# Performance work log

Measured on AMD Instinct MI355X. Metric: run time of the kernel, lower is better.

## Reference

```python
import jax, jax.numpy as jnp
import numpy as np

# Module config: RoDAlignMax(aligned_height=9, aligned_width=9, spatial_scale=0.25)
# Internally RoDAlignFunction is called with aligned_height+1, aligned_width+1,
# then max_pool2d(kernel=2, stride=1) shrinks each spatial dim by 1.
AH, AW = 10, 10          # pre-pool sampling grid (aligned_{h,w} + 1)
SPATIAL_SCALE = 0.25


def _rod_align(features, rois, ah, aw, scale):
    """RoDAlign: uniform bilinear sampling grid over the WHOLE feature map,
    with samples falling INSIDE the ROI zeroed out (region-of-discard).
    features: [B,C,H,W], rois: [R,5]=(batch_ind,x1,y1,x2,y2) -> [R,C,ah,aw]."""
    B, C, H, W = features.shape
    dt = features.dtype
    bidx = rois[:, 0].astype(jnp.int32)                              # [R]
    x1 = rois[:, 1] * scale
    y1 = rois[:, 2] * scale
    x2 = rois[:, 3] * scale
    y2 = rois[:, 4] * scale
    # uniform grid spanning the full feature map
    h = jnp.arange(ah, dtype=dt) * ((H - 1.0) / (ah - 1.0))          # [AH]
    w = jnp.arange(aw, dtype=dt) * ((W - 1.0) / (aw - 1.0))          # [AW]
    h0 = jnp.minimum(jnp.floor(h), H - 2).astype(jnp.int32)
    w0 = jnp.minimum(jnp.floor(w), W - 2).astype(jnp.int32)
    hr = (h - h0.astype(dt))[:, None, None]                          # [AH,1,1]
    wr = (w - w0.astype(dt))[None, :, None]                          # [1,AW,1]
    b = bidx[:, None, None]                                          # [R,1,1]
    hi0 = h0[None, :, None]; hi1 = hi0 + 1                           # [1,AH,1]
    wi0 = w0[None, None, :]; wi1 = wi0 + 1                           # [1,1,AW]
    # four corner gathers; advanced idx dims go first -> [R,AH,AW,C]
    ul = features[b, :, hi0, wi0]
    ur = features[b, :, hi0, wi1]
    dl = features[b, :, hi1, wi0]
    dr = features[b, :, hi1, wi1]
    out = (ul * (1 - hr) * (1 - wr) + ur * (1 - hr) * wr
           + dl * hr * (1 - wr) + dr * hr * wr)                      # [R,AH,AW,C]
    # zero samples inside the ROI (the kept crop region is discarded)
    in_h = (h[None, :] >= y1[:, None]) & (h[None, :] <= y2[:, None])  # [R,AH]
    in_w = (w[None, :] >= x1[:, None]) & (w[None, :] <= x2[:, None])  # [R,AW]
    inside = in_h[:, :, None] & in_w[:, None, :]                      # [R,AH,AW]
    out = jnp.where(inside[..., None], jnp.zeros((), dt), out)
    return jnp.transpose(out, (0, 3, 1, 2))                           # [R,C,AH,AW]


def _maxpool2x2_s1(x):
    # max_pool2d(kernel_size=2, stride=1) on [..., H, W]
    return jnp.maximum(jnp.maximum(x[..., :-1, :-1], x[..., :-1, 1:]),
                       jnp.maximum(x[..., 1:, :-1], x[..., 1:, 1:]))


def setup_inputs() -> dict:
    key = jax.random.key(0)
    k1, k2, k3, k4, k5 = jax.random.split(key, 5)
    B, C, H, W = 4, 256, 64, 64
    R = 2048
    img = H / SPATIAL_SCALE  # 256.0, input-image coordinate extent
    features = jax.random.normal(k1, (B, C, H, W), dtype=jnp.float32)
    bidx = jax.random.randint(k2, (R,), 0, B).astype(jnp.float32)
    x1 = jax.random.uniform(k3, (R,), dtype=jnp.float32) * (img * 0.5)
    y1 = jax.random.uniform(k4, (R,), dtype=jnp.float32) * (img * 0.5)
    wh = jax.random.uniform(k5, (R, 2), dtype=jnp.float32) * (img * 0.45) + img * 0.05
    x2 = jnp.minimum(x1 + wh[:, 0], img - 1.0)
    y2 = jnp.minimum(y1 + wh[:, 1], img - 1.0)
    rois = jnp.stack([bidx, x1, y1, x2, y2], axis=1)  # [R,5]
    return {"features": features, "rois": rois}


def reference(features, rois):
    x = _rod_align(features, rois, AH, AW, SPATIAL_SCALE)  # [R,C,10,10]
    return _maxpool2x2_s1(x)                               # [R,C,9,9]
```

## Files before the change

### kernel.cpp

```cpp
#include <hip/hip_runtime.h>


#define NB 4
#define NC 256
#define HW 64
#define NR 2048

__global__ __launch_bounds__(256) void rod_gather(const float* __restrict__ F,
                                                  float* __restrict__ G) {
    int idx = blockIdx.x * 256 + threadIdx.x;
    int c = idx & 255;
    int t = idx >> 8;
    int p = t % 100;
    int b = t / 100;
    int i = p / 10, j = p - i * 10;
    G[idx] = F[((b * NC + c) << 12) + i * 448 + j * 7];
}

__global__ __launch_bounds__(128) void rod_main(const float* __restrict__ G,
                                                const float* __restrict__ rois,
                                                float* __restrict__ out) {
    __shared__ float lds[128 * 83];
    const int tid  = threadIdx.x;
    const int r    = blockIdx.x >> 1;
    const int half = blockIdx.x & 1;
    const int c    = half * 128 + tid;

    const float x1 = rois[r * 5 + 1] * 0.25f;
    const float y1 = rois[r * 5 + 2] * 0.25f;
    const float x2 = rois[r * 5 + 3] * 0.25f;
    const float y2 = rois[r * 5 + 4] * 0.25f;
    const int  b   = (int)rois[r * 5 + 0];

    bool inw[10], inh[10];
    #pragma unroll
    for (int j = 0; j < 10; ++j) {
        float s = 7.0f * (float)j;
        inw[j] = (s >= x1) && (s <= x2);
        inh[j] = (s >= y1) && (s <= y2);
    }

    const float* gb = G + (size_t)b * 100 * NC + c;

    float vprev[10];
    #pragma unroll
    for (int j = 0; j < 10; ++j) {
        float g = gb[j * NC];
        vprev[j] = (inh[0] && inw[j]) ? 0.0f : g;
    }
    #pragma unroll
    for (int i = 1; i < 10; ++i) {
        float vcur[10];
        #pragma unroll
        for (int j = 0; j < 10; ++j) {
            float g = gb[(i * 10 + j) * NC];
            vcur[j] = (inh[i] && inw[j]) ? 0.0f : g;
        }
        float rm[10];
        #pragma unroll
        for (int j = 0; j < 10; ++j) rm[j] = fmaxf(vprev[j], vcur[j]);
        #pragma unroll
        for (int j = 0; j < 9; ++j)
            lds[tid * 83 + (i - 1) * 9 + j] = fmaxf(rm[j], rm[j + 1]);
        #pragma unroll
        for (int j = 0; j < 10; ++j) vprev[j] = vcur[j];
    }
    __syncthreads();

    float* dst = out + (size_t)r * 20736 + half * 10368;
    #pragma unroll 9
    for (int k = 0; k < 81; ++k) {
        int el = tid + (k << 7);
        int cc = (int)((unsigned)el / 81u);
        dst[el] = lds[el + cc * 2];
    }
}

extern "C" void kernel_launch(void* const* d_in, const int* in_sizes, int n_in,
                              void* d_out, int out_size, void* d_ws, size_t ws_size,
                              hipStream_t stream) {
    const float* F    = (const float*)d_in[0];
    const float* rois = (const float*)d_in[1];
    float*       out  = (float*)d_out;
    float*       G    = (float*)d_ws;

    rod_gather<<<dim3(400), dim3(256), 0, stream>>>(F, G);
    rod_main<<<dim3(NR * 2), dim3(128), 0, stream>>>(G, rois, out);
}
```

Measured before the change: 184.8 us.

## Use channel-major gathered grid and compute outputs directly in output order

The gather stage now stores the 10x10 sample grid per (batch, channel) contiguously rather than channel-innermost. The main kernel drops the LDS transpose and the barrier. Each thread computes output elements in their final linear order, reading four neighbouring grid samples straight from global or cache memory and applying bitmask-based ROI zeroing. This removes shared-memory staging, but each output now does four scattered loads instead of reusing values held in registers.

```diff
diff --git a/kernel.cpp b/kernel.cpp
--- a/kernel.cpp
+++ b/kernel.cpp
@@ -1,78 +1,68 @@
 #include <hip/hip_runtime.h>
 
 
-#define NB 4
 #define NC 256
-#define HW 64
 #define NR 2048
 
-__global__ __launch_bounds__(256) void rod_gather(const float* __restrict__ F,
-                                                  float* __restrict__ G) {
-    int idx = blockIdx.x * 256 + threadIdx.x;
-    int c = idx & 255;
-    int t = idx >> 8;
-    int p = t % 100;
-    int b = t / 100;
-    int i = p / 10, j = p - i * 10;
-    G[idx] = F[((b * NC + c) << 12) + i * 448 + j * 7];
+__global__ __launch_bounds__(128) void rod_gather2(const float* __restrict__ F,
+                                                   float* __restrict__ G2) {
+    int bc = blockIdx.x;
+    int t  = threadIdx.x;
+    if (t < 100) {
+        int i = (t * 205) >> 11;
+        int j = t - 10 * i;
+        G2[bc * 100 + t] = F[(bc << 12) + i * 448 + j * 7];
+    }
 }
 
-__global__ __launch_bounds__(128) void rod_main(const float* __restrict__ G,
-                                                const float* __restrict__ rois,
-                                                float* __restrict__ out) {
-    __shared__ float lds[128 * 83];
-    const int tid  = threadIdx.x;
-    const int r    = blockIdx.x >> 1;
-    const int half = blockIdx.x & 1;
-    const int c    = half * 128 + tid;
+__global__ __launch_bounds__(256, 4) void rod_main2(const float* __restrict__ G2,
+                                                    const float* __restrict__ rois,
+                                                    float* __restrict__ out) {
+    const int tid = threadIdx.x;
+    const int r   = blockIdx.x;
 
     const float x1 = rois[r * 5 + 1] * 0.25f;
     const float y1 = rois[r * 5 + 2] * 0.25f;
     const float x2 = rois[r * 5 + 3] * 0.25f;
     const float y2 = rois[r * 5 + 4] * 0.25f;
-    const int  b   = (int)rois[r * 5 + 0];
+    const int   b  = (int)rois[r * 5 + 0];
 
-    bool inw[10], inh[10];
+    unsigned inhM = 0u, inwM = 0u;
     #pragma unroll
-    for (int j = 0; j < 10; ++j) {
-        float s = 7.0f * (float)j;
-        inw[j] = (s >= x1) && (s <= x2);
-        inh[j] = (s >= y1) && (s <= y2);
+    for (int t = 0; t < 10; ++t) {
+        float s = 7.0f * (float)t;
+        if ((s >= y1) && (s <= y2)) inhM |= (1u << t);
+        if ((s >= x1) && (s <= x2)) inwM |= (1u << t);
     }
 
-    const float* gb = G + (size_t)b * 100 * NC + c;
+    const float* Gb  = G2 + b * 25600;
+    float*       dst = out + (size_t)r * 20736;
 
-    float vprev[10];
-    #pragma unroll
-    for (int j = 0; j < 10; ++j) {
-        float g = gb[j * NC];
-        vprev[j] = (inh[0] && inw[j]) ? 0.0f : g;
-    }
-    #pragma unroll
-    for (int i = 1; i < 10; ++i) {
-        float vcur[10];
-        #pragma unroll
-        for (int j = 0; j < 10; ++j) {
-            float g = gb[(i * 10 + j) * NC];
-            vcur[j] = (inh[i] && inw[j]) ? 0.0f : g;
-        }
-        float rm[10];
-        #pragma unroll
-        for (int j = 0; j < 10; ++j) rm[j] = fmaxf(vprev[j], vcur[j]);
-        #pragma unroll
-        for (int j = 0; j < 9; ++j)
-            lds[tid * 83 + (i - 1) * 9 + j] = fmaxf(rm[j], rm[j + 1]);
-        #pragma unroll
-        for (int j = 0; j < 10; ++j) vprev[j] = vcur[j];
-    }
-    __syncthreads();
+    int c = (tid * 405) >> 15;
+    int q = tid - 81 * c;
 
-    float* dst = out + (size_t)r * 20736 + half * 10368;
-    #pragma unroll 9
+    #pragma unroll 4
     for (int k = 0; k < 81; ++k) {
-        int el = tid + (k << 7);
-        int cc = (int)((unsigned)el / 81u);
-        dst[el] = lds[el + cc * 2];
+        int i = (q * 57) >> 9;
+        int j = q - 9 * i;
+
+        const float* gp = Gb + c * 100 + i * 10 + j;
+        float v00 = gp[0];
+        float v01 = gp[1];
+        float v10 = gp[10];
+        float v11 = gp[11];
+
+        unsigned hb = inhM >> i;
+        unsigned wb = inwM >> j;
+        float a00 = ((hb        & wb       ) & 1u) ? 0.0f : v00;
+        float a01 = ((hb        & (wb >> 1)) & 1u) ? 0.0f : v01;
+        float a10 = (((hb >> 1) & wb       ) & 1u) ? 0.0f : v10;
+        float a11 = (((hb >> 1) & (wb >> 1)) & 1u) ? 0.0f : v11;
+
+        dst[tid + (k << 8)] = fmaxf(fmaxf(a00, a01), fmaxf(a10, a11));
+
+        q += 13; c += 3;
+        if (q >= 81) { q -= 81; c += 1; }
     }
 }
 
@@ -82,8 +72,8 @@
     const float* F    = (const float*)d_in[0];
     const float* rois = (const float*)d_in[1];
     float*       out  = (float*)d_out;
-    float*       G    = (float*)d_ws;
+    float*       G2   = (float*)d_ws;
 
-    rod_gather<<<dim3(400), dim3(256), 0, stream>>>(F, G);
-    rod_main<<<dim3(NR * 2), dim3(128), 0, stream>>>(G, rois, out);
+    rod_gather2<<<dim3(1024), dim3(128), 0, stream>>>(F, G2);
+    rod_main2<<<dim3(NR), dim3(256), 0, stream>>>(G2, rois, out);
 }
```

After: 195.0 us. +5.5%, slower.
